# Optimization experiments

Hardware: AMD Instinct MI355X
Metric: run time of the kernel (lower is better)

The kernel has to match this reference:

```python
import jax, jax.numpy as jnp
import numpy as np

EMB = 512
HEADS = 8

def setup_inputs() -> dict:
    key = jax.random.key(0)
    ks = jax.random.split(key, 6)
    x = jax.random.normal(ks[0], (8, 1024, EMB), dtype=jnp.float32)
    s = EMB ** -0.5
    Wq = jax.random.normal(ks[1], (EMB, EMB), dtype=jnp.float32) * s
    Wk = jax.random.normal(ks[2], (EMB, EMB), dtype=jnp.float32) * s
    Wv = jax.random.normal(ks[3], (EMB, EMB), dtype=jnp.float32) * s
    ln_gamma = jnp.ones((EMB,), dtype=jnp.float32)
    ln_beta = jnp.zeros((EMB,), dtype=jnp.float32)
    return {"x": x, "Wq": Wq, "Wk": Wk, "Wv": Wv, "ln_gamma": ln_gamma, "ln_beta": ln_beta}

def reference(x, Wq, Wk, Wv, ln_gamma, ln_beta):
    B, S, E = x.shape
    H = HEADS
    D = E // H
    scale = E ** -0.5  # note: source scales by emb_size**-0.5, not head_dim
    # projections (bias=False, torch Linear: x @ W.T)
    q = (x @ Wq.T).reshape(B, S, H, D).transpose(0, 2, 1, 3)  # [B,H,S,D]
    k = (x @ Wk.T).reshape(B, S, H, D).transpose(0, 2, 1, 3)
    v = (x @ Wv.T).reshape(B, S, H, D).transpose(0, 2, 1, 3)
    attn = jnp.einsum('bhqd,bhkd->bhqk', q, k) * scale
    attn = jax.nn.softmax(attn, axis=-1)
    out = jnp.einsum('bhqk,bhkd->bhqd', attn, v)
    out = out.transpose(0, 2, 1, 3).reshape(B, S, E)
    # LayerNorm (eps=1e-5, torch default)
    mu = jnp.mean(out, axis=-1, keepdims=True)
    var = jnp.var(out, axis=-1, keepdims=True)
    out = (out - mu) * jax.lax.rsqrt(var + 1e-5) * ln_gamma + ln_beta
    return out
```

## Files before the change

### kernel.cpp

```cpp
#include <hip/hip_runtime.h>
#include <hip/hip_bf16.h>

typedef __bf16 bf16_t;
typedef __bf16 bf16x4 __attribute__((ext_vector_type(4)));
typedef __bf16 bf16x8 __attribute__((ext_vector_type(8)));
typedef float  f32x4  __attribute__((ext_vector_type(4)));
typedef short  short4v __attribute__((ext_vector_type(4)));

#define GLL(gp, lp) __builtin_amdgcn_global_load_lds((const __attribute__((address_space(1))) void*)(gp), (__attribute__((address_space(3))) void*)(lp), 16, 0, 0)

__device__ __forceinline__ f32x4 mfma16x16x16_bf16(bf16x4 a, bf16x4 b, f32x4 c) {
#if __has_builtin(__builtin_amdgcn_mfma_f32_16x16x16_bf16)
    return __builtin_amdgcn_mfma_f32_16x16x16_bf16(a, b, c, 0, 0, 0);
#else
    return __builtin_amdgcn_mfma_f32_16x16x16bf16_1k(__builtin_bit_cast(short4v, a), __builtin_bit_cast(short4v, b), c, 0, 0, 0);
#endif
}

__device__ __forceinline__ float fexp2(float x) {
#if __has_builtin(__builtin_amdgcn_exp2f)
    return __builtin_amdgcn_exp2f(x);
#else
    return exp2f(x);
#endif
}

__global__ __launch_bounds__(256) void cvt_kernel(const float* __restrict__ x,
                                                  const float* __restrict__ wq,
                                                  const float* __restrict__ wk,
                                                  const float* __restrict__ wv,
                                                  bf16_t* __restrict__ xb,
                                                  bf16_t* __restrict__ wall) {
    const int TOT4 = 1245184;
    for (int i = blockIdx.x * blockDim.x + threadIdx.x; i < TOT4; i += gridDim.x * blockDim.x) {
        const float* src; bf16_t* dst; int off;
        if (i < 1048576) { src = x; dst = xb; off = i; }
        else {
            int j = i - 1048576;
            int wsel = j >> 16;
            off = j & 65535;
            src = (wsel == 0) ? wq : ((wsel == 1) ? wk : wv);
            dst = wall + ((size_t)wsel << 18);
        }
        float4 v = *(const float4*)(src + (size_t)off * 4);
        bf16x4 o = { (bf16_t)v.x, (bf16_t)v.y, (bf16_t)v.z, (bf16_t)v.w };
        *(bf16x4*)(dst + (size_t)off * 4) = o;
    }
}

__global__ __launch_bounds__(256) void proj_kernel(const bf16_t* __restrict__ xb,
                                                   const bf16_t* __restrict__ wall,
                                                   bf16_t* __restrict__ Qb,
                                                   bf16_t* __restrict__ Kb,
                                                   bf16_t* __restrict__ Vt) {
    __shared__ char psm[34816];

    const int tid = threadIdx.x;
    const int w = tid >> 6, lane = tid & 63;
    const int bx = blockIdx.x;
    const int nb = bx % 12, mb = bx / 12;
    const int n0 = nb * 128, m0 = mb * 128;
    const int wn = w & 1, wm = w >> 1;
    const int l15 = lane & 15, g = lane >> 4;

    const int srow = w * 32 + (lane >> 2);
    const int kcol = (lane & 3) * 8;
    const bf16_t* wsrc0 = wall + (size_t)(n0 + srow) * 512 + kcol;
    const bf16_t* xsrc0 = xb + (size_t)(m0 + srow) * 512 + kcol;

    f32x4 acc[4][4] = {};

    {
        bf16_t* lw = (bf16_t*)(psm) + w * 1024;
        bf16_t* lx = (bf16_t*)(psm + 8192) + w * 1024;
        GLL(wsrc0, lw);
        GLL(wsrc0 + 8192, lw + 512);
        GLL(xsrc0, lx);
        GLL(xsrc0 + 8192, lx + 512);
    }
    __syncthreads();

    for (int kt = 0; kt < 16; ++kt) {
        const int buf = kt & 1;
        if (kt < 15) {
            const int ko = (kt + 1) * 32;
            bf16_t* lw = (bf16_t*)(psm + (buf ^ 1) * 16384) + w * 1024;
            bf16_t* lx = (bf16_t*)(psm + (buf ^ 1) * 16384 + 8192) + w * 1024;
            GLL(wsrc0 + ko, lw);
            GLL(wsrc0 + 8192 + ko, lw + 512);
            GLL(xsrc0 + ko, lx);
            GLL(xsrc0 + 8192 + ko, lx + 512);
        }
        const bf16_t* sW = (const bf16_t*)(psm + buf * 16384);
        const bf16_t* sX = (const bf16_t*)(psm + buf * 16384 + 8192);

        bf16x8 af[4], bfv[4];
#pragma unroll
        for (int ni = 0; ni < 4; ++ni)
            af[ni] = *(const bf16x8*)(sW + (wn * 64 + ni * 16 + l15) * 32 + g * 8);
#pragma unroll
        for (int mi = 0; mi < 4; ++mi)
            bfv[mi] = *(const bf16x8*)(sX + (wm * 64 + mi * 16 + l15) * 32 + g * 8);
#pragma unroll
        for (int ni = 0; ni < 4; ++ni)
#pragma unroll
            for (int mi = 0; mi < 4; ++mi)
                acc[ni][mi] = __builtin_amdgcn_mfma_f32_16x16x32_bf16(af[ni], bfv[mi], acc[ni][mi], 0, 0, 0);
        __syncthreads();
    }

    const int which = n0 >> 9;
    if (which < 2) {
        bf16_t* dst = (which == 0) ? Qb : Kb;
#pragma unroll
        for (int ni = 0; ni < 4; ++ni) {
#pragma unroll
            for (int mi = 0; mi < 4; ++mi) {
                int j = (n0 & 511) + wn * 64 + ni * 16 + g * 4;
                int h = j >> 6, dd = j & 63;
                int sb = m0 + wm * 64 + mi * 16 + l15;
                int b = sb >> 10, s = sb & 1023;
                bf16x4 o = { (bf16_t)acc[ni][mi][0], (bf16_t)acc[ni][mi][1],
                             (bf16_t)acc[ni][mi][2], (bf16_t)acc[ni][mi][3] };
                *(bf16x4*)(dst + ((size_t)((b * 8 + h) * 1024 + s)) * 64 + dd) = o;
            }
        }
    } else {
        bf16_t* ctile = (bf16_t*)psm;
#pragma unroll
        for (int ni = 0; ni < 4; ++ni)
#pragma unroll
            for (int mi = 0; mi < 4; ++mi)
#pragma unroll
                for (int r = 0; r < 4; ++r)
                    ctile[(wn * 64 + ni * 16 + g * 4 + r) * 136 + wm * 64 + mi * 16 + l15] =
                        (bf16_t)acc[ni][mi][r];
        __syncthreads();
        const int rr = tid >> 1, half = tid & 1;
        const int jv = (n0 & 511) + rr;
        const int hh = jv >> 6, dd = jv & 63;
        const int b = m0 >> 10, sb = (m0 & 1023) + half * 64;
        bf16_t* dst = Vt + ((size_t)((b * 8 + hh) * 64 + dd)) * 1024 + sb;
        const bf16_t* src = ctile + rr * 136 + half * 64;
#pragma unroll
        for (int u = 0; u < 8; ++u)
            *(bf16x8*)(dst + u * 8) = *(const bf16x8*)(src + u * 8);
    }
}

__global__ __launch_bounds__(512, 2) void attn_kernel(const bf16_t* __restrict__ Qb,
                                                      const bf16_t* __restrict__ Kb,
                                                      const bf16_t* __restrict__ Vt,
                                                      bf16_t* __restrict__ Ob) {
    __shared__ char smK[65536];
    __shared__ char smV[65536];
    const int tid = threadIdx.x;
    const int w = tid >> 6, lane = tid & 63;
    const int l15 = lane & 15, g = lane >> 4, l7 = lane & 7;

    const int bx = blockIdx.x;
    const int head = bx & 63;
    const int qq = bx >> 6;
    const int q0 = qq * 256 + w * 32;

    const size_t hoff = (size_t)head << 16;
    const bf16_t* Qh = Qb + hoff;
    const char* Kh = (const char*)(Kb + hoff);
    const char* Vh = (const char*)(Vt + hoff);

    const float c2 = 0.06376390597f;

    const char* KsrcT = Kh + (tid >> 3) * 128 + (((tid & 7) ^ ((tid >> 3) & 7)) << 4);
    const char* VsrcT = Vh + (size_t)w * 2048 + ((lane ^ w) << 4);
    char* KdstT = smK + (w << 10);
    char* VdstT = smV + (w << 10);

#pragma unroll
    for (int c = 0; c < 8; ++c) GLL(KsrcT + c * 8192, KdstT + c * 8192);
#pragma unroll
    for (int c = 0; c < 8; ++c) GLL(VsrcT + c * 16384, VdstT + c * 8192);

    bf16x8 qf[2][2];
#pragma unroll
    for (int qh = 0; qh < 2; ++qh) {
        const bf16_t* qp = Qh + (q0 + qh * 16 + l15) * 64 + g * 8;
        bf16x8 a = *(const bf16x8*)(qp);
        bf16x8 bq = *(const bf16x8*)(qp + 32);
#pragma unroll
        for (int j = 0; j < 8; ++j) {
            a[j] = (bf16_t)((float)a[j] * c2);
            bq[j] = (bf16_t)((float)bq[j] * c2);
        }
        qf[qh][0] = a; qf[qh][1] = bq;
    }

    f32x4 oacc[2][4] = {};
    f32x4 dacc[2] = {};
    const bf16x4 ones = { (bf16_t)1.0f, (bf16_t)1.0f, (bf16_t)1.0f, (bf16_t)1.0f };
    const f32x4 minit = { -4.0f, -4.0f, -4.0f, -4.0f };

    const int ke0 = (g ^ l7) << 4;

    __syncthreads();

#pragma unroll 1
    for (int phase = 0; phase < 2; ++phase) {
#pragma unroll 2
        for (int sub = 0; sub < 32; ++sub) {
            const char* krp = smK + (sub * 16 + l15) * 128;
            bf16x8 ka0 = *(const bf16x8*)(krp + ke0);
            bf16x8 ka1 = *(const bf16x8*)(krp + (ke0 ^ 64));
            bf16x4 pb[2];
#pragma unroll
            for (int qh = 0; qh < 2; ++qh) {
                f32x4 st = __builtin_amdgcn_mfma_f32_16x16x32_bf16(ka0, qf[qh][0], minit, 0, 0, 0);
                st = __builtin_amdgcn_mfma_f32_16x16x32_bf16(ka1, qf[qh][1], st, 0, 0, 0);
                bf16x4 pv = { (bf16_t)fexp2(st[0]), (bf16_t)fexp2(st[1]),
                              (bf16_t)fexp2(st[2]), (bf16_t)fexp2(st[3]) };
                pb[qh] = pv;
                dacc[qh] = mfma16x16x16_bf16(ones, pv, dacc[qh]);
            }
            const int vcol = (((sub * 2 + (g >> 1)) ^ l7) << 4) + ((g & 1) << 3);
#pragma unroll
            for (int dt = 0; dt < 4; ++dt) {
                bf16x4 va = *(const bf16x4*)(smV + (dt * 16 + l15) * 1024 + vcol);
                oacc[0][dt] = mfma16x16x16_bf16(va, pb[0], oacc[0][dt]);
                oacc[1][dt] = mfma16x16x16_bf16(va, pb[1], oacc[1][dt]);
            }
        }
        if (phase == 0) {
            __syncthreads();
#pragma unroll
            for (int c = 0; c < 8; ++c) GLL(KsrcT + 65536 + c * 8192, KdstT + c * 8192);
#pragma unroll
            for (int c = 0; c < 8; ++c) GLL(VsrcT + 1024 + c * 16384, VdstT + c * 8192);
            __syncthreads();
        }
    }

    const int b = head >> 3, h = head & 7;
#pragma unroll
    for (int qh = 0; qh < 2; ++qh) {
        const float inv = 1.0f / dacc[qh][0];
        const int s = q0 + qh * 16 + l15;
        bf16_t* op = Ob + ((size_t)(b * 1024 + s)) * 512 + h * 64 + g * 4;
#pragma unroll
        for (int dt = 0; dt < 4; ++dt) {
            bf16x4 o = { (bf16_t)(oacc[qh][dt][0] * inv), (bf16_t)(oacc[qh][dt][1] * inv),
                         (bf16_t)(oacc[qh][dt][2] * inv), (bf16_t)(oacc[qh][dt][3] * inv) };
            *(bf16x4*)(op + dt * 16) = o;
        }
    }
}

__global__ __launch_bounds__(256) void ln_kernel(const bf16_t* __restrict__ O,
                                                 const float* __restrict__ gamma,
                                                 const float* __restrict__ beta,
                                                 float* __restrict__ out) {
    const int w = threadIdx.x >> 6, lane = threadIdx.x & 63;
    const int row = blockIdx.x * 4 + w;
    const bf16_t* rp = O + (size_t)row * 512 + lane * 8;
    bf16x8 v8 = *(const bf16x8*)rp;
    float v[8];
    float sum = 0.0f, sq = 0.0f;
#pragma unroll
    for (int i = 0; i < 8; ++i) { v[i] = (float)v8[i]; sum += v[i]; sq += v[i] * v[i]; }
#pragma unroll
    for (int msk = 1; msk < 64; msk <<= 1) {
        sum += __shfl_xor(sum, msk);
        sq  += __shfl_xor(sq, msk);
    }
    const float mean = sum * (1.0f / 512.0f);
    const float var = sq * (1.0f / 512.0f) - mean * mean;
    const float rs = rsqrtf(var + 1e-5f);
    float4 g0 = *(const float4*)(gamma + lane * 8);
    float4 g1 = *(const float4*)(gamma + lane * 8 + 4);
    float4 b0 = *(const float4*)(beta + lane * 8);
    float4 b1 = *(const float4*)(beta + lane * 8 + 4);
    float* op = out + (size_t)row * 512 + lane * 8;
    float4 o0, o1;
    o0.x = (v[0] - mean) * rs * g0.x + b0.x;
    o0.y = (v[1] - mean) * rs * g0.y + b0.y;
    o0.z = (v[2] - mean) * rs * g0.z + b0.z;
    o0.w = (v[3] - mean) * rs * g0.w + b0.w;
    o1.x = (v[4] - mean) * rs * g1.x + b1.x;
    o1.y = (v[5] - mean) * rs * g1.y + b1.y;
    o1.z = (v[6] - mean) * rs * g1.z + b1.z;
    o1.w = (v[7] - mean) * rs * g1.w + b1.w;
    *(float4*)op = o0;
    *(float4*)(op + 4) = o1;
}

extern "C" void kernel_launch(void* const* d_in, const int* in_sizes, int n_in,
                              void* d_out, int out_size, void* d_ws, size_t ws_size,
                              hipStream_t stream) {
    const float* x  = (const float*)d_in[0];
    const float* wq = (const float*)d_in[1];
    const float* wk = (const float*)d_in[2];
    const float* wv = (const float*)d_in[3];
    const float* gamma = (const float*)d_in[4];
    const float* beta  = (const float*)d_in[5];
    float* out = (float*)d_out;

    char* ws = (char*)d_ws;
    bf16_t* xb   = (bf16_t*)(ws);
    bf16_t* wall = (bf16_t*)(ws + 8388608);
    bf16_t* Qb   = (bf16_t*)(ws + 9961472);
    bf16_t* Kb   = (bf16_t*)(ws + 18350080);
    bf16_t* Vt   = (bf16_t*)(ws + 26738688);
    bf16_t* Ob   = (bf16_t*)(ws + 35127296);

    hipLaunchKernelGGL(cvt_kernel,  dim3(1024), dim3(256), 0, stream, x, wq, wk, wv, xb, wall);
    hipLaunchKernelGGL(proj_kernel, dim3(768),  dim3(256), 0, stream, xb, wall, Qb, Kb, Vt);
    hipLaunchKernelGGL(attn_kernel, dim3(256),  dim3(512), 0, stream, Qb, Kb, Vt, Ob);
    hipLaunchKernelGGL(ln_kernel,   dim3(2048), dim3(256), 0, stream, Ob, gamma, beta, out);
}
```

Before: 65.92 us.

## Fuse convert, projection, attention and layernorm into one cooperative persistent kernel

Replaces the four separate kernel launches with a single cooperative kernel of 256 blocks of 512 threads, separated by grid-wide syncs. The projection GEMM is remapped so each block handles three 128x128 tiles with a 4x2 warp layout, and the layernorm loops over four row groups per block. This removes launch gaps and inter-kernel tail effects, but adds grid-sync costs and forces every phase to run at the attention kernel's block size and occupancy. It also caps the grid at 256 blocks, which may reduce parallelism in the projection and convert phases.

After: 176.4 us. +167.7%, slower.

```diff
diff --git a/kernel.cpp b/kernel.cpp
--- a/kernel.cpp
+++ b/kernel.cpp
@@ -1,5 +1,8 @@
 #include <hip/hip_runtime.h>
+#include <hip/hip_cooperative_groups.h>
 #include <hip/hip_bf16.h>
+
+namespace cg = cooperative_groups;
 
 typedef __bf16 bf16_t;
 typedef __bf16 bf16x4 __attribute__((ext_vector_type(4)));
@@ -25,14 +28,24 @@
 #endif
 }
 
-__global__ __launch_bounds__(256) void cvt_kernel(const float* __restrict__ x,
-                                                  const float* __restrict__ wq,
-                                                  const float* __restrict__ wk,
-                                                  const float* __restrict__ wv,
-                                                  bf16_t* __restrict__ xb,
-                                                  bf16_t* __restrict__ wall) {
-    const int TOT4 = 1245184;
-    for (int i = blockIdx.x * blockDim.x + threadIdx.x; i < TOT4; i += gridDim.x * blockDim.x) {
+__global__ __launch_bounds__(512, 2) void mega_kernel(
+    const float* __restrict__ x, const float* __restrict__ wq,
+    const float* __restrict__ wk, const float* __restrict__ wv,
+    const float* __restrict__ gamma, const float* __restrict__ beta,
+    float* __restrict__ out,
+    bf16_t* __restrict__ xb, bf16_t* __restrict__ wall,
+    bf16_t* __restrict__ Qb, bf16_t* __restrict__ Kb,
+    bf16_t* __restrict__ Vt, bf16_t* __restrict__ Ob)
+{
+    __shared__ char smem[131072];
+    cg::grid_group grid = cg::this_grid();
+
+    const int tid = threadIdx.x;
+    const int bx = blockIdx.x;
+    const int w = tid >> 6, lane = tid & 63;
+    const int l15 = lane & 15, g = lane >> 4, l7 = lane & 7;
+
+    for (int i = bx * 512 + tid; i < 1245184; i += 131072) {
         const float* src; bf16_t* dst; int off;
         if (i < 1048576) { src = x; dst = xb; off = i; }
         else {
@@ -46,249 +59,222 @@
         bf16x4 o = { (bf16_t)v.x, (bf16_t)v.y, (bf16_t)v.z, (bf16_t)v.w };
         *(bf16x4*)(dst + (size_t)off * 4) = o;
     }
-}
-
-__global__ __launch_bounds__(256) void proj_kernel(const bf16_t* __restrict__ xb,
-                                                   const bf16_t* __restrict__ wall,
-                                                   bf16_t* __restrict__ Qb,
-                                                   bf16_t* __restrict__ Kb,
-                                                   bf16_t* __restrict__ Vt) {
-    __shared__ char psm[34816];
-
-    const int tid = threadIdx.x;
-    const int w = tid >> 6, lane = tid & 63;
-    const int bx = blockIdx.x;
-    const int nb = bx % 12, mb = bx / 12;
-    const int n0 = nb * 128, m0 = mb * 128;
-    const int wn = w & 1, wm = w >> 1;
-    const int l15 = lane & 15, g = lane >> 4;
-
-    const int srow = w * 32 + (lane >> 2);
-    const int kcol = (lane & 3) * 8;
-    const bf16_t* wsrc0 = wall + (size_t)(n0 + srow) * 512 + kcol;
-    const bf16_t* xsrc0 = xb + (size_t)(m0 + srow) * 512 + kcol;
-
-    f32x4 acc[4][4] = {};
-
-    {
-        bf16_t* lw = (bf16_t*)(psm) + w * 1024;
-        bf16_t* lx = (bf16_t*)(psm + 8192) + w * 1024;
-        GLL(wsrc0, lw);
-        GLL(wsrc0 + 8192, lw + 512);
-        GLL(xsrc0, lx);
-        GLL(xsrc0 + 8192, lx + 512);
-    }
-    __syncthreads();
-
-    for (int kt = 0; kt < 16; ++kt) {
-        const int buf = kt & 1;
-        if (kt < 15) {
-            const int ko = (kt + 1) * 32;
-            bf16_t* lw = (bf16_t*)(psm + (buf ^ 1) * 16384) + w * 1024;
-            bf16_t* lx = (bf16_t*)(psm + (buf ^ 1) * 16384 + 8192) + w * 1024;
-            GLL(wsrc0 + ko, lw);
-            GLL(wsrc0 + 8192 + ko, lw + 512);
-            GLL(xsrc0 + ko, lx);
-            GLL(xsrc0 + 8192 + ko, lx + 512);
-        }
-        const bf16_t* sW = (const bf16_t*)(psm + buf * 16384);
-        const bf16_t* sX = (const bf16_t*)(psm + buf * 16384 + 8192);
-
-        bf16x8 af[4], bfv[4];
-#pragma unroll
-        for (int ni = 0; ni < 4; ++ni)
-            af[ni] = *(const bf16x8*)(sW + (wn * 64 + ni * 16 + l15) * 32 + g * 8);
-#pragma unroll
-        for (int mi = 0; mi < 4; ++mi)
-            bfv[mi] = *(const bf16x8*)(sX + (wm * 64 + mi * 16 + l15) * 32 + g * 8);
-#pragma unroll
-        for (int ni = 0; ni < 4; ++ni)
-#pragma unroll
-            for (int mi = 0; mi < 4; ++mi)
-                acc[ni][mi] = __builtin_amdgcn_mfma_f32_16x16x32_bf16(af[ni], bfv[mi], acc[ni][mi], 0, 0, 0);
+    grid.sync();
+
+    for (int rep = 0; rep < 3; ++rep) {
+        const int t = rep * 256 + bx;
+        const int nb = t % 12, mb = t / 12;
+        const int n0 = nb * 128, m0 = mb * 128;
+        const int wn = w & 1, wm = w >> 1;
+
+        const bf16_t* wsrc0 = wall + (size_t)(n0 + (tid >> 2)) * 512 + (tid & 3) * 8;
+        const bf16_t* xsrc0 = xb + (size_t)(m0 + (tid >> 2)) * 512 + (tid & 3) * 8;
+
+        f32x4 acc[4][2] = {};
+
+        GLL(wsrc0, smem + w * 1024);
+        GLL(xsrc0, smem + 8192 + w * 1024);
+        __syncthreads();
+
+        for (int kt = 0; kt < 16; ++kt) {
+            const int buf = kt & 1;
+            if (kt < 15) {
+                const int ko = (kt + 1) * 32;
+                GLL(wsrc0 + ko, smem + (buf ^ 1) * 16384 + w * 1024);
+                GLL(xsrc0 + ko, smem + (buf ^ 1) * 16384 + 8192 + w * 1024);
+            }
+            const bf16_t* sW = (const bf16_t*)(smem + buf * 16384);
+            const bf16_t* sX = (const bf16_t*)(smem + buf * 16384 + 8192);
+
+            bf16x8 af[4], bfv[2];
+#pragma unroll
+            for (int ni = 0; ni < 4; ++ni)
+                af[ni] = *(const bf16x8*)(sW + (wn * 64 + ni * 16 + l15) * 32 + g * 8);
+#pragma unroll
+            for (int mi = 0; mi < 2; ++mi)
+                bfv[mi] = *(const bf16x8*)(sX + (wm * 32 + mi * 16 + l15) * 32 + g * 8);
+#pragma unroll
+            for (int ni = 0; ni < 4; ++ni)
+#pragma unroll
+                for (int mi = 0; mi < 2; ++mi)
+                    acc[ni][mi] = __builtin_amdgcn_mfma_f32_16x16x32_bf16(af[ni], bfv[mi], acc[ni][mi], 0, 0, 0);
+            __syncthreads();
+        }
+
+        const int which = n0 >> 9;
+        if (which < 2) {
+            bf16_t* dst = (which == 0) ? Qb : Kb;
+#pragma unroll
+            for (int ni = 0; ni < 4; ++ni) {
+#pragma unroll
+                for (int mi = 0; mi < 2; ++mi) {
+                    int j = (n0 & 511) + wn * 64 + ni * 16 + g * 4;
+                    int h = j >> 6, dd = j & 63;
+                    int sb = m0 + wm * 32 + mi * 16 + l15;
+                    int b = sb >> 10, s = sb & 1023;
+                    bf16x4 o = { (bf16_t)acc[ni][mi][0], (bf16_t)acc[ni][mi][1],
+                                 (bf16_t)acc[ni][mi][2], (bf16_t)acc[ni][mi][3] };
+                    *(bf16x4*)(dst + ((size_t)((b * 8 + h) * 1024 + s)) * 64 + dd) = o;
+                }
+            }
+        } else {
+            bf16_t* ctile = (bf16_t*)smem;
+#pragma unroll
+            for (int ni = 0; ni < 4; ++ni)
+#pragma unroll
+                for (int mi = 0; mi < 2; ++mi)
+#pragma unroll
+                    for (int r = 0; r < 4; ++r)
+                        ctile[(wn * 64 + ni * 16 + g * 4 + r) * 136 + wm * 32 + mi * 16 + l15] =
+                            (bf16_t)acc[ni][mi][r];
+            __syncthreads();
+            const int rr = tid >> 2, qtr = tid & 3;
+            const int jv = (n0 & 511) + rr;
+            const int hh = jv >> 6, dd = jv & 63;
+            const int b = m0 >> 10, sb = (m0 & 1023) + qtr * 32;
+            bf16_t* dst = Vt + ((size_t)((b * 8 + hh) * 64 + dd)) * 1024 + sb;
+            const bf16_t* src = ctile + rr * 136 + qtr * 32;
+#pragma unroll
+            for (int u = 0; u < 4; ++u)
+                *(bf16x8*)(dst + u * 8) = *(const bf16x8*)(src + u * 8);
+        }
         __syncthreads();
     }
-
-    const int which = n0 >> 9;
-    if (which < 2) {
-        bf16_t* dst = (which == 0) ? Qb : Kb;
-#pragma unroll
-        for (int ni = 0; ni < 4; ++ni) {
-#pragma unroll
-            for (int mi = 0; mi < 4; ++mi) {
-                int j = (n0 & 511) + wn * 64 + ni * 16 + g * 4;
-                int h = j >> 6, dd = j & 63;
-                int sb = m0 + wm * 64 + mi * 16 + l15;
-                int b = sb >> 10, s = sb & 1023;
-                bf16x4 o = { (bf16_t)acc[ni][mi][0], (bf16_t)acc[ni][mi][1],
-                             (bf16_t)acc[ni][mi][2], (bf16_t)acc[ni][mi][3] };
-                *(bf16x4*)(dst + ((size_t)((b * 8 + h) * 1024 + s)) * 64 + dd) = o;
-            }
-        }
-    } else {
-        bf16_t* ctile = (bf16_t*)psm;
-#pragma unroll
-        for (int ni = 0; ni < 4; ++ni)
-#pragma unroll
-            for (int mi = 0; mi < 4; ++mi)
-#pragma unroll
-                for (int r = 0; r < 4; ++r)
-                    ctile[(wn * 64 + ni * 16 + g * 4 + r) * 136 + wm * 64 + mi * 16 + l15] =
-                        (bf16_t)acc[ni][mi][r];
+    grid.sync();
+
+    {
+        char* smK = smem;
+        char* smV = smem + 65536;
+
+        const int head = bx & 63;
+        const int qq = bx >> 6;
+        const int q0 = qq * 256 + w * 32;
+
+        const size_t hoff = (size_t)head << 16;
+        const bf16_t* Qh = Qb + hoff;
+        const char* Kh = (const char*)(Kb + hoff);
+        const char* Vh = (const char*)(Vt + hoff);
+
+        const float c2 = 0.06376390597f;
+
+        const char* KsrcT = Kh + (tid >> 3) * 128 + (((tid & 7) ^ ((tid >> 3) & 7)) << 4);
+        const char* VsrcT = Vh + (size_t)w * 2048 + ((lane ^ w) << 4);
+        char* KdstT = smK + (w << 10);
+        char* VdstT = smV + (w << 10);
+
+#pragma unroll
+        for (int c = 0; c < 8; ++c) GLL(KsrcT + c * 8192, KdstT + c * 8192);
+#pragma unroll
+        for (int c = 0; c < 8; ++c) GLL(VsrcT + c * 16384, VdstT + c * 8192);
+
+        bf16x8 qf[2][2];
+#pragma unroll
+        for (int qh = 0; qh < 2; ++qh) {
+            const bf16_t* qp = Qh + (q0 + qh * 16 + l15) * 64 + g * 8;
+            bf16x8 a = *(const bf16x8*)(qp);
+            bf16x8 bq = *(const bf16x8*)(qp + 32);
+#pragma unroll
+            for (int j = 0; j < 8; ++j) {
+                a[j] = (bf16_t)((float)a[j] * c2);
+                bq[j] = (bf16_t)((float)bq[j] * c2);
+            }
+            qf[qh][0] = a; qf[qh][1] = bq;
+        }
+
+        f32x4 oacc[2][4] = {};
+        f32x4 dacc[2] = {};
+        const bf16x4 ones = { (bf16_t)1.0f, (bf16_t)1.0f, (bf16_t)1.0f, (bf16_t)1.0f };
+        const f32x4 minit = { -4.0f, -4.0f, -4.0f, -4.0f };
+
+        const int ke0 = (g ^ l7) << 4;
+
         __syncthreads();
-        const int rr = tid >> 1, half = tid & 1;
-        const int jv = (n0 & 511) + rr;
-        const int hh = jv >> 6, dd = jv & 63;
-        const int b = m0 >> 10, sb = (m0 & 1023) + half * 64;
-        bf16_t* dst = Vt + ((size_t)((b * 8 + hh) * 64 + dd)) * 1024 + sb;
-        const bf16_t* src = ctile + rr * 136 + half * 64;
-#pragma unroll
-        for (int u = 0; u < 8; ++u)
-            *(bf16x8*)(dst + u * 8) = *(const bf16x8*)(src + u * 8);
+
+#pragma unroll 1
+        for (int phase = 0; phase < 2; ++phase) {
+#pragma unroll 2
+            for (int sub = 0; sub < 32; ++sub) {
+                const char* krp = smK + (sub * 16 + l15) * 128;
+                bf16x8 ka0 = *(const bf16x8*)(krp + ke0);
+                bf16x8 ka1 = *(const bf16x8*)(krp + (ke0 ^ 64));
+                bf16x4 pb[2];
+#pragma unroll
+                for (int qh = 0; qh < 2; ++qh) {
+                    f32x4 st = __builtin_amdgcn_mfma_f32_16x16x32_bf16(ka0, qf[qh][0], minit, 0, 0, 0);
+                    st = __builtin_amdgcn_mfma_f32_16x16x32_bf16(ka1, qf[qh][1], st, 0, 0, 0);
+                    bf16x4 pv = { (bf16_t)fexp2(st[0]), (bf16_t)fexp2(st[1]),
+                                  (bf16_t)fexp2(st[2]), (bf16_t)fexp2(st[3]) };
+                    pb[qh] = pv;
+                    dacc[qh] = mfma16x16x16_bf16(ones, pv, dacc[qh]);
+                }
+                const int vcol = (((sub * 2 + (g >> 1)) ^ l7) << 4) + ((g & 1) << 3);
+#pragma unroll
+                for (int dt = 0; dt < 4; ++dt) {
+                    bf16x4 va = *(const bf16x4*)(smV + (dt * 16 + l15) * 1024 + vcol);
+                    oacc[0][dt] = mfma16x16x16_bf16(va, pb[0], oacc[0][dt]);
+                    oacc[1][dt] = mfma16x16x16_bf16(va, pb[1], oacc[1][dt]);
+                }
+            }
+            if (phase == 0) {
+                __syncthreads();
+#pragma unroll
+                for (int c = 0; c < 8; ++c) GLL(KsrcT + 65536 + c * 8192, KdstT + c * 8192);
+#pragma unroll
+                for (int c = 0; c < 8; ++c) GLL(VsrcT + 1024 + c * 16384, VdstT + c * 8192);
+                __syncthreads();
+            }
+        }
+
+        const int b = head >> 3, h = head & 7;
+#pragma unroll
+        for (int qh = 0; qh < 2; ++qh) {
+            const float inv = 1.0f / dacc[qh][0];
+            const int s = q0 + qh * 16 + l15;
+            bf16_t* op = Ob + ((size_t)(b * 1024 + s)) * 512 + h * 64 + g * 4;
+#pragma unroll
+            for (int dt = 0; dt < 4; ++dt) {
+                bf16x4 o = { (bf16_t)(oacc[qh][dt][0] * inv), (bf16_t)(oacc[qh][dt][1] * inv),
+                             (bf16_t)(oacc[qh][dt][2] * inv), (bf16_t)(oacc[qh][dt][3] * inv) };
+                *(bf16x4*)(op + dt * 16) = o;
+            }
+        }
     }
-}
-
-__global__ __launch_bounds__(512, 2) void attn_kernel(const bf16_t* __restrict__ Qb,
-                                                      const bf16_t* __restrict__ Kb,
-                                                      const bf16_t* __restrict__ Vt,
-                                                      bf16_t* __restrict__ Ob) {
-    __shared__ char smK[65536];
-    __shared__ char smV[65536];
-    const int tid = threadIdx.x;
-    const int w = tid >> 6, lane = tid & 63;
-    const int l15 = lane & 15, g = lane >> 4, l7 = lane & 7;
-
-    const int bx = blockIdx.x;
-    const int head = bx & 63;
-    const int qq = bx >> 6;
-    const int q0 = qq * 256 + w * 32;
-
-    const size_t hoff = (size_t)head << 16;
-    const bf16_t* Qh = Qb + hoff;
-    const char* Kh = (const char*)(Kb + hoff);
-    const char* Vh = (const char*)(Vt + hoff);
-
-    const float c2 = 0.06376390597f;
-
-    const char* KsrcT = Kh + (tid >> 3) * 128 + (((tid & 7) ^ ((tid >> 3) & 7)) << 4);
-    const char* VsrcT = Vh + (size_t)w * 2048 + ((lane ^ w) << 4);
-    char* KdstT = smK + (w << 10);
-    char* VdstT = smV + (w << 10);
-
-#pragma unroll
-    for (int c = 0; c < 8; ++c) GLL(KsrcT + c * 8192, KdstT + c * 8192);
-#pragma unroll
-    for (int c = 0; c < 8; ++c) GLL(VsrcT + c * 16384, VdstT + c * 8192);
-
-    bf16x8 qf[2][2];
-#pragma unroll
-    for (int qh = 0; qh < 2; ++qh) {
-        const bf16_t* qp = Qh + (q0 + qh * 16 + l15) * 64 + g * 8;
-        bf16x8 a = *(const bf16x8*)(qp);
-        bf16x8 bq = *(const bf16x8*)(qp + 32);
-#pragma unroll
-        for (int j = 0; j < 8; ++j) {
-            a[j] = (bf16_t)((float)a[j] * c2);
-            bq[j] = (bf16_t)((float)bq[j] * c2);
-        }
-        qf[qh][0] = a; qf[qh][1] = bq;
+    grid.sync();
+
+#pragma unroll 1
+    for (int r = 0; r < 4; ++r) {
+        const int row = bx * 32 + r * 8 + w;
+        const bf16_t* rp = Ob + (size_t)row * 512 + lane * 8;
+        bf16x8 v8 = *(const bf16x8*)rp;
+        float v[8];
+        float sum = 0.0f, sq = 0.0f;
+#pragma unroll
+        for (int i = 0; i < 8; ++i) { v[i] = (float)v8[i]; sum += v[i]; sq += v[i] * v[i]; }
+#pragma unroll
+        for (int msk = 1; msk < 64; msk <<= 1) {
+            sum += __shfl_xor(sum, msk);
+            sq  += __shfl_xor(sq, msk);
+        }
+        const float mean = sum * (1.0f / 512.0f);
+        const float var = sq * (1.0f / 512.0f) - mean * mean;
+        const float rs = rsqrtf(var + 1e-5f);
+        float4 g0 = *(const float4*)(gamma + lane * 8);
+        float4 g1 = *(const float4*)(gamma + lane * 8 + 4);
+        float4 b0 = *(const float4*)(beta + lane * 8);
+        float4 b1 = *(const float4*)(beta + lane * 8 + 4);
+        float* op = out + (size_t)row * 512 + lane * 8;
+        float4 o0, o1;
+        o0.x = (v[0] - mean) * rs * g0.x + b0.x;
+        o0.y = (v[1] - mean) * rs * g0.y + b0.y;
+        o0.z = (v[2] - mean) * rs * g0.z + b0.z;
+        o0.w = (v[3] - mean) * rs * g0.w + b0.w;
+        o1.x = (v[4] - mean) * rs * g1.x + b1.x;
+        o1.y = (v[5] - mean) * rs * g1.y + b1.y;
+        o1.z = (v[6] - mean) * rs * g1.z + b1.z;
+        o1.w = (v[7] - mean) * rs * g1.w + b1.w;
+        *(float4*)op = o0;
+        *(float4*)(op + 4) = o1;
     }
-
-    f32x4 oacc[2][4] = {};
-    f32x4 dacc[2] = {};
-    const bf16x4 ones = { (bf16_t)1.0f, (bf16_t)1.0f, (bf16_t)1.0f, (bf16_t)1.0f };
-    const f32x4 minit = { -4.0f, -4.0f, -4.0f, -4.0f };
-
-    const int ke0 = (g ^ l7) << 4;
-
-    __syncthreads();
-
-#pragma unroll 1
-    for (int phase = 0; phase < 2; ++phase) {
-#pragma unroll 2
-        for (int sub = 0; sub < 32; ++sub) {
-            const char* krp = smK + (sub * 16 + l15) * 128;
-            bf16x8 ka0 = *(const bf16x8*)(krp + ke0);
-            bf16x8 ka1 = *(const bf16x8*)(krp + (ke0 ^ 64));
-            bf16x4 pb[2];
-#pragma unroll
-            for (int qh = 0; qh < 2; ++qh) {
-                f32x4 st = __builtin_amdgcn_mfma_f32_16x16x32_bf16(ka0, qf[qh][0], minit, 0, 0, 0);
-                st = __builtin_amdgcn_mfma_f32_16x16x32_bf16(ka1, qf[qh][1], st, 0, 0, 0);
-                bf16x4 pv = { (bf16_t)fexp2(st[0]), (bf16_t)fexp2(st[1]),
-                              (bf16_t)fexp2(st[2]), (bf16_t)fexp2(st[3]) };
-                pb[qh] = pv;
-                dacc[qh] = mfma16x16x16_bf16(ones, pv, dacc[qh]);
-            }
-            const int vcol = (((sub * 2 + (g >> 1)) ^ l7) << 4) + ((g & 1) << 3);
-#pragma unroll
-            for (int dt = 0; dt < 4; ++dt) {
-                bf16x4 va = *(const bf16x4*)(smV + (dt * 16 + l15) * 1024 + vcol);
-                oacc[0][dt] = mfma16x16x16_bf16(va, pb[0], oacc[0][dt]);
-                oacc[1][dt] = mfma16x16x16_bf16(va, pb[1], oacc[1][dt]);
-            }
-        }
-        if (phase == 0) {
-            __syncthreads();
-#pragma unroll
-            for (int c = 0; c < 8; ++c) GLL(KsrcT + 65536 + c * 8192, KdstT + c * 8192);
-#pragma unroll
-            for (int c = 0; c < 8; ++c) GLL(VsrcT + 1024 + c * 16384, VdstT + c * 8192);
-            __syncthreads();
-        }
-    }
-
-    const int b = head >> 3, h = head & 7;
-#pragma unroll
-    for (int qh = 0; qh < 2; ++qh) {
-        const float inv = 1.0f / dacc[qh][0];
-        const int s = q0 + qh * 16 + l15;
-        bf16_t* op = Ob + ((size_t)(b * 1024 + s)) * 512 + h * 64 + g * 4;
-#pragma unroll
-        for (int dt = 0; dt < 4; ++dt) {
-            bf16x4 o = { (bf16_t)(oacc[qh][dt][0] * inv), (bf16_t)(oacc[qh][dt][1] * inv),
-                         (bf16_t)(oacc[qh][dt][2] * inv), (bf16_t)(oacc[qh][dt][3] * inv) };
-            *(bf16x4*)(op + dt * 16) = o;
-        }
-    }
-}
-
-__global__ __launch_bounds__(256) void ln_kernel(const bf16_t* __restrict__ O,
-                                                 const float* __restrict__ gamma,
-                                                 const float* __restrict__ beta,
-                                                 float* __restrict__ out) {
-    const int w = threadIdx.x >> 6, lane = threadIdx.x & 63;
-    const int row = blockIdx.x * 4 + w;
-    const bf16_t* rp = O + (size_t)row * 512 + lane * 8;
-    bf16x8 v8 = *(const bf16x8*)rp;
-    float v[8];
-    float sum = 0.0f, sq = 0.0f;
-#pragma unroll
-    for (int i = 0; i < 8; ++i) { v[i] = (float)v8[i]; sum += v[i]; sq += v[i] * v[i]; }
-#pragma unroll
-    for (int msk = 1; msk < 64; msk <<= 1) {
-        sum += __shfl_xor(sum, msk);
-        sq  += __shfl_xor(sq, msk);
-    }
-    const float mean = sum * (1.0f / 512.0f);
-    const float var = sq * (1.0f / 512.0f) - mean * mean;
-    const float rs = rsqrtf(var + 1e-5f);
-    float4 g0 = *(const float4*)(gamma + lane * 8);
-    float4 g1 = *(const float4*)(gamma + lane * 8 + 4);
-    float4 b0 = *(const float4*)(beta + lane * 8);
-    float4 b1 = *(const float4*)(beta + lane * 8 + 4);
-    float* op = out + (size_t)row * 512 + lane * 8;
-    float4 o0, o1;
-    o0.x = (v[0] - mean) * rs * g0.x + b0.x;
-    o0.y = (v[1] - mean) * rs * g0.y + b0.y;
-    o0.z = (v[2] - mean) * rs * g0.z + b0.z;
-    o0.w = (v[3] - mean) * rs * g0.w + b0.w;
-    o1.x = (v[4] - mean) * rs * g1.x + b1.x;
-    o1.y = (v[5] - mean) * rs * g1.y + b1.y;
-    o1.z = (v[6] - mean) * rs * g1.z + b1.z;
-    o1.w = (v[7] - mean) * rs * g1.w + b1.w;
-    *(float4*)op = o0;
-    *(float4*)(op + 4) = o1;
 }
 
 extern "C" void kernel_launch(void* const* d_in, const int* in_sizes, int n_in,
@@ -310,8 +296,9 @@
     bf16_t* Vt   = (bf16_t*)(ws + 26738688);
     bf16_t* Ob   = (bf16_t*)(ws + 35127296);
 
-    hipLaunchKernelGGL(cvt_kernel,  dim3(1024), dim3(256), 0, stream, x, wq, wk, wv, xb, wall);
-    hipLaunchKernelGGL(proj_kernel, dim3(768),  dim3(256), 0, stream, xb, wall, Qb, Kb, Vt);
-    hipLaunchKernelGGL(attn_kernel, dim3(256),  dim3(512), 0, stream, Qb, Kb, Vt, Ob);
-    hipLaunchKernelGGL(ln_kernel,   dim3(2048), dim3(256), 0, stream, Ob, gamma, beta, out);
+    void* args[] = { (void*)&x, (void*)&wq, (void*)&wk, (void*)&wv,
+                     (void*)&gamma, (void*)&beta, (void*)&out,
+                     (void*)&xb, (void*)&wall, (void*)&Qb, (void*)&Kb,
+                     (void*)&Vt, (void*)&Ob };
+    hipLaunchCooperativeKernel((void*)mega_kernel, dim3(256), dim3(512), args, 0, stream);
 }
```
